# Kernel optimization log

Measured on AMD Instinct MI355X. Metric: run time of the kernel, lower is better.

Reference implementation:

```python
import jax, jax.numpy as jnp
import numpy as np

B, C, T, N = 8, 64, 24, 512
H = 2
D = C // H  # 32
NEG = -1e9
LN_EPS = 1e-5


def setup_inputs() -> dict:
    key = jax.random.key(0)
    ks = jax.random.split(key, 8)
    s = 1.0 / np.sqrt(C)
    return {
        "x": jax.random.normal(ks[0], (B, C, T, N), jnp.float32),
        "gso": jax.random.randint(ks[1], (N, N), 0, 2, jnp.int32),
        "Wq": jax.random.normal(ks[2], (C, C), jnp.float32) * s,
        "Wk": jax.random.normal(ks[3], (C, C), jnp.float32) * s,
        "Wv": jax.random.normal(ks[4], (C, C), jnp.float32) * s,
        "a_src": jax.random.normal(ks[5], (H, D), jnp.float32) * s,
        "a_dst": jax.random.normal(ks[6], (H, D), jnp.float32) * s,
        "gamma": jnp.ones((C,), jnp.float32),
        "beta": jnp.zeros((C,), jnp.float32),
    }


def reference(x, gso, Wq, Wk, Wv, a_src, a_dst, gamma, beta):
    # x: (B, C, T, N) -> (M, N, C) with M = B*T
    xr = jnp.transpose(x, (0, 2, 3, 1)).reshape(B * T, N, C)
    # torch Linear: y = x @ W.T ; split heads -> (M, N, H, D)
    Q = jnp.einsum('mnc,dc->mnd', xr, Wq).reshape(B * T, N, H, D)
    K = jnp.einsum('mnc,dc->mnd', xr, Wk).reshape(B * T, N, H, D)
    V = jnp.einsum('mnc,dc->mnd', xr, Wv).reshape(B * T, N, H, D)
    # additive GAT scores: s_ij = leaky_relu(<q_i, a_src> + <k_j, a_dst>)
    s_src = jnp.einsum('mnhd,hd->mhn', Q, a_src)  # (M, H, N)
    s_dst = jnp.einsum('mnhd,hd->mhn', K, a_dst)  # (M, H, N)
    scores = s_src[:, :, :, None] + s_dst[:, :, None, :]  # (M, H, N, N)
    scores = jax.nn.leaky_relu(scores, negative_slope=0.2)
    mask = jnp.where(gso == 0, jnp.float32(NEG), jnp.float32(0.0))  # (N, N)
    scores = scores + mask[None, None, :, :]
    attn = jax.nn.softmax(scores, axis=-1)  # dropout is identity in eval
    out = jnp.einsum('mhij,mjhd->mihd', attn, V).reshape(B * T, N, C)
    # LayerNorm over channels
    mu = jnp.mean(out, axis=-1, keepdims=True)
    var = jnp.var(out, axis=-1, keepdims=True)
    out = (out - mu) * jax.lax.rsqrt(var + LN_EPS) * gamma + beta
    # (M, N, C) -> (B, C, T, N)
    return jnp.transpose(out.reshape(B, T, N, C), (0, 3, 1, 2))
```

## Files before the change

### kernel.cpp

```cpp
#include <hip/hip_runtime.h>
#include <hip/hip_bf16.h>


#define NB 8
#define NC 64
#define NT 24
#define NN 512
#define NM 192
#define LOG2E 1.44269504088896f
#define NEGBIG -1.0e9f

typedef float f32x4 __attribute__((ext_vector_type(4)));
typedef short bf16x8 __attribute__((ext_vector_type(8)));
typedef int   i32x4 __attribute__((ext_vector_type(4)));
typedef unsigned int u32;
typedef u32 u32x2 __attribute__((ext_vector_type(2)));

#ifndef __has_builtin
#define __has_builtin(x) 0
#endif

__device__ __forceinline__ float fast_exp2(float x) {
#if __has_builtin(__builtin_amdgcn_exp2f)
    return __builtin_amdgcn_exp2f(x);
#else
    return exp2f(x);
#endif
}

__device__ __forceinline__ unsigned short f2bf(float f) {
    union { float f; unsigned int u; } v; v.f = f;
    unsigned int u = v.u;
    u += 0x7fffu + ((u >> 16) & 1u);
    return (unsigned short)(u >> 16);
}

__device__ __forceinline__ u32 pk_bf16(float lo, float hi) {
    __hip_bfloat162 h2 = __float22bfloat162_rn(float2{lo, hi});
    u32 r; __builtin_memcpy(&r, &h2, 4); return r;
}
__device__ __forceinline__ unsigned short f2bfh(float f) {
    __hip_bfloat16 h = __float2bfloat16(f);
    unsigned short r; __builtin_memcpy(&r, &h, 2); return r;
}

__device__ __forceinline__ float bf2f(unsigned short s) {
    union { unsigned int u; float f; } v;
    v.u = ((unsigned int)s) << 16;
    return v.f;
}

#define VT2_IDX(k2,h,qq,dt,dl,e) \
    ((((((k2)*2+(h))*4+(qq))*2+(dt))*16+(dl))*8+(e))

#define XRB(n,c) (((n)<<6) + (((((c)>>3) ^ ((n)&7))<<3) | ((c)&7)))

#define VT_IDX(h,k,qq,dt,dl,e) ((((((h)*16+(k))*4+(qq))*2+(dt))*16+(dl))*8+(e))

#define WS_VT_OFF   0u
#define WS_SSRC_OFF 12582912u
#define WS_SDST_OFF 13369344u
#define WS_MASK_OFF 14155776u
#define WS_NEEDED   15204352u

__global__ __launch_bounds__(512)
void gat_proj(const float* __restrict__ x, const int* __restrict__ gso,
              const float* __restrict__ Wq, const float* __restrict__ Wk,
              const float* __restrict__ Wv, const float* __restrict__ a_src,
              const float* __restrict__ a_dst,
              unsigned short* __restrict__ vt_ws, float* __restrict__ ssrc_ws,
              float* __restrict__ sdst_ws, float* __restrict__ mask_ws)
{
    __shared__ unsigned short sm_xrb[8192];
    __shared__ unsigned short sm_wvb[4096];
    __shared__ float sm_wqa[2][NC];
    __shared__ float sm_wka[2][NC];

    const int bid  = blockIdx.x;
    const int m    = bid >> 2;
    const int ch   = bid & 3;
    const int b    = m / NT;
    const int tt   = m % NT;
    const int tid  = threadIdx.x;
    const int lane = tid & 63;
    const int wid  = tid >> 6;
    const int fr   = lane & 15;
    const int fq   = lane >> 4;

    if (bid < 16) {
        const int w  = bid * 512 + tid;
        const int i  = w >> 4, kk = w & 15;
        const int* gp = &gso[i * NN + kk * 32];
        float* mp = &mask_ws[i * NN + kk * 32];
        #pragma unroll
        for (int q = 0; q < 8; ++q) {
            const i32x4 g = *reinterpret_cast<const i32x4*>(gp + q * 4);
            f32x4 f;
            #pragma unroll
            for (int e = 0; e < 4; ++e) f[e] = (g[e] != 0) ? 0.f : NEGBIG;
            *reinterpret_cast<f32x4*>(mp + q * 4) = f;
        }
    }

    if (tid < 128) {
        const int h = tid >> 6, c = tid & 63;
        float aq = 0.f, ak = 0.f;
        #pragma unroll
        for (int d = 0; d < 32; ++d) {
            aq += Wq[(h*32 + d)*NC + c] * a_src[h*32 + d];
            ak += Wk[(h*32 + d)*NC + c] * a_dst[h*32 + d];
        }
        sm_wqa[h][c] = aq * LOG2E;
        sm_wka[h][c] = ak * LOG2E;
    }
    for (int idx = tid; idx < 4096; idx += 512) {
        const int e   = idx & 7;
        const int dl  = (idx >> 3) & 15;
        const int dt4 = (idx >> 7) & 3;
        const int qq  = (idx >> 9) & 3;
        const int ks  = idx >> 11;
        sm_wvb[idx] = f2bfh(Wv[(dt4*16 + dl)*NC + ks*32 + qq*8 + e]);
    }

    const int nbase = ch * 128;

    {
        const int sl = tid & 127;
        const int sc = tid >> 7;
        #pragma unroll
        for (int half = 0; half < 2; ++half) {
            float v[8];
            #pragma unroll
            for (int e = 0; e < 8; ++e) {
                const int c = sc*16 + half*8 + e;
                v[e] = x[((size_t)(b*NC + c)*NT + tt)*NN + nbase + sl];
            }
            i32x4 w;
            #pragma unroll
            for (int j = 0; j < 4; ++j)
                w[j] = (int)pk_bf16(v[2*j], v[2*j+1]);
            *reinterpret_cast<i32x4*>(&sm_xrb[XRB(sl, sc*16 + half*8)]) = w;
        }
    }
    __syncthreads();

    {
        const int nl = tid >> 2;
        const int pp = tid & 3;
        float sq0=0.f, sq1=0.f, sk0=0.f, sk1=0.f;
        #pragma unroll
        for (int cc = 0; cc < 16; ++cc) {
            const int c = pp*16 + cc;
            const float xv = bf2f(sm_xrb[XRB(nl, c)]);
            sq0 += xv * sm_wqa[0][c];
            sq1 += xv * sm_wqa[1][c];
            sk0 += xv * sm_wka[0][c];
            sk1 += xv * sm_wka[1][c];
        }
        sq0 += __shfl_xor(sq0,1); sq0 += __shfl_xor(sq0,2);
        sq1 += __shfl_xor(sq1,1); sq1 += __shfl_xor(sq1,2);
        sk0 += __shfl_xor(sk0,1); sk0 += __shfl_xor(sk0,2);
        sk1 += __shfl_xor(sk1,1); sk1 += __shfl_xor(sk1,2);
        if (pp == 0) {
            ssrc_ws[((size_t)m*2 + 0)*NN + nbase + nl] = sq0;
            ssrc_ws[((size_t)m*2 + 1)*NN + nbase + nl] = sq1;
            sdst_ws[((size_t)m*2 + 0)*NN + nbase + nl] = sk0;
            sdst_ws[((size_t)m*2 + 1)*NN + nbase + nl] = sk1;
        }
    }

    {
        f32x4 vacc[4] = {};
        #pragma unroll
        for (int ks = 0; ks < 2; ++ks) {
            const bf16x8 af = *reinterpret_cast<const bf16x8*>(
                &sm_xrb[XRB(wid*16 + fr, ks*32 + fq*8)]);
            #pragma unroll
            for (int dt4 = 0; dt4 < 4; ++dt4) {
                const bf16x8 bfv = *reinterpret_cast<const bf16x8*>(
                    &sm_wvb[(((ks*4 + fq)*4 + dt4)*16 + fr)*8]);
                vacc[dt4] = __builtin_amdgcn_mfma_f32_16x16x32_bf16(
                    af, bfv, vacc[dt4], 0, 0, 0);
            }
        }
        const int n0 = nbase + wid*16 + 4*fq;
        #pragma unroll
        for (int dt4 = 0; dt4 < 4; ++dt4) {
            const int h = dt4 >> 1, dt = dt4 & 1;
            u32x2 dd;
            dd[0] = pk_bf16(vacc[dt4][0], vacc[dt4][1]);
            dd[1] = pk_bf16(vacc[dt4][2], vacc[dt4][3]);
            *reinterpret_cast<u32x2*>(
                &vt_ws[(size_t)m*32768 +
                       VT2_IDX(n0>>5, h, (n0>>3)&3, dt, fr, n0&7)]) = dd;
        }
    }
}

__global__ __launch_bounds__(512, 8)
void gat_attn(const unsigned short* __restrict__ vt_ws,
              const float* __restrict__ ssrc_ws, const float* __restrict__ sdst_ws,
              const float* __restrict__ mask_ws,
              const float* __restrict__ gamma, const float* __restrict__ beta,
              float* __restrict__ out)
{
    __shared__ unsigned short sm_vt[16384];
    __shared__ float sm_sdst[2][NN];
    __shared__ float sm_ssrc[2][128];

    const int bid  = blockIdx.x;
    const int m    = (bid >> 5) * 8 + (bid & 7);
    const int ch   = (bid >> 3) & 3;
    const int tid  = threadIdx.x;
    const int lane = tid & 63;
    const int wid  = tid >> 6;
    const int fr   = lane & 15;
    const int fq   = lane >> 4;

    const char* vsrc = (const char*)(vt_ws + (size_t)m * 32768);
#if __has_builtin(__builtin_amdgcn_global_load_lds)
    #pragma unroll
    for (int i = 0; i < 4; ++i) {
        __builtin_amdgcn_global_load_lds(
            (const __attribute__((address_space(1))) void*)
                (vsrc + i*8192 + tid*16),
            (__attribute__((address_space(3))) void*)
                (((__attribute__((address_space(3))) char*)sm_vt) +
                 i*8192 + (tid & ~63)*16),
            16, 0, 0);
    }
#else
    #pragma unroll
    for (int i = 0; i < 4; ++i) {
        reinterpret_cast<i32x4*>(sm_vt)[i*512 + tid] =
            reinterpret_cast<const i32x4*>(vsrc)[i*512 + tid];
    }
#endif
    if (tid < 256) {
        reinterpret_cast<f32x4*>(&sm_sdst[0][0])[tid] =
            reinterpret_cast<const f32x4*>(sdst_ws + (size_t)m*2*NN)[tid];
    } else {
        const int t = tid - 256;
        const int h = t >> 7, nloc = t & 127;
        sm_ssrc[h][nloc] = ssrc_ws[((size_t)m*2 + h)*NN + ch*128 + nloc];
    }
    __syncthreads();

    bf16x8 bones;
    {
        union { i32x4 i; bf16x8 h; } cv;
        const int w = (fr == 0) ? 0x3F803F80 : 0;
        cv.i[0] = w; cv.i[1] = w; cv.i[2] = w; cv.i[3] = w;
        bones = cv.h;
    }

    const int iloc = wid * 16;
    const int ig   = ch*128 + iloc + fr;
    const float src0 = sm_ssrc[0][iloc + fr];
    const float src1 = sm_ssrc[1][iloc + fr];
    const float* mrow = mask_ws + (size_t)ig * NN + fq*8;

    f32x4 acc[4] = {};
    f32x4 accs0 = {}, accs1 = {};

    #pragma unroll
    for (int hf = 0; hf < 2; ++hf) {
        #pragma unroll 4
        for (int k2 = 0; k2 < 8; ++k2) {
            const int k  = hf*8 + k2;
            const int j0 = k*32 + fq*8;
            const float* mp = mrow + k*32;
            const f32x4 ma = *reinterpret_cast<const f32x4*>(mp);
            const f32x4 mb = *reinterpret_cast<const f32x4*>(mp + 4);

            {
                const f32x4 da = *reinterpret_cast<const f32x4*>(&sm_sdst[0][j0]);
                const f32x4 db = *reinterpret_cast<const f32x4*>(&sm_sdst[0][j0+4]);
                u32 u[8];
                #pragma unroll
                for (int e = 0; e < 4; ++e) {
                    float sc = src0 + da[e] + ma[e];
                    sc = fmaxf(sc, 0.2f*sc);
                    u[e] = __float_as_uint(fast_exp2(sc));
                }
                #pragma unroll
                for (int e = 0; e < 4; ++e) {
                    float sc = src0 + db[e] + mb[e];
                    sc = fmaxf(sc, 0.2f*sc);
                    u[4+e] = __float_as_uint(fast_exp2(sc));
                }
                union { i32x4 i; bf16x8 h; } cv;
                cv.i[0] = __builtin_amdgcn_perm(u[1], u[0], 0x07060302u);
                cv.i[1] = __builtin_amdgcn_perm(u[3], u[2], 0x07060302u);
                cv.i[2] = __builtin_amdgcn_perm(u[5], u[4], 0x07060302u);
                cv.i[3] = __builtin_amdgcn_perm(u[7], u[6], 0x07060302u);
                const bf16x8 af = cv.h;
                accs0 = __builtin_amdgcn_mfma_f32_16x16x32_bf16(af, bones, accs0, 0,0,0);
                const bf16x8 b0 = *reinterpret_cast<const bf16x8*>(
                    &sm_vt[VT2_IDX(k2,0,fq,0,fr,0)]);
                const bf16x8 b1 = *reinterpret_cast<const bf16x8*>(
                    &sm_vt[VT2_IDX(k2,0,fq,1,fr,0)]);
                acc[0] = __builtin_amdgcn_mfma_f32_16x16x32_bf16(af, b0, acc[0], 0,0,0);
                acc[1] = __builtin_amdgcn_mfma_f32_16x16x32_bf16(af, b1, acc[1], 0,0,0);
            }
            {
                const f32x4 da = *reinterpret_cast<const f32x4*>(&sm_sdst[1][j0]);
                const f32x4 db = *reinterpret_cast<const f32x4*>(&sm_sdst[1][j0+4]);
                u32 u[8];
                #pragma unroll
                for (int e = 0; e < 4; ++e) {
                    float sc = src1 + da[e] + ma[e];
                    sc = fmaxf(sc, 0.2f*sc);
                    u[e] = __float_as_uint(fast_exp2(sc));
                }
                #pragma unroll
                for (int e = 0; e < 4; ++e) {
                    float sc = src1 + db[e] + mb[e];
                    sc = fmaxf(sc, 0.2f*sc);
                    u[4+e] = __float_as_uint(fast_exp2(sc));
                }
                union { i32x4 i; bf16x8 h; } cv;
                cv.i[0] = __builtin_amdgcn_perm(u[1], u[0], 0x07060302u);
                cv.i[1] = __builtin_amdgcn_perm(u[3], u[2], 0x07060302u);
                cv.i[2] = __builtin_amdgcn_perm(u[5], u[4], 0x07060302u);
                cv.i[3] = __builtin_amdgcn_perm(u[7], u[6], 0x07060302u);
                const bf16x8 af = cv.h;
                accs1 = __builtin_amdgcn_mfma_f32_16x16x32_bf16(af, bones, accs1, 0,0,0);
                const bf16x8 b0 = *reinterpret_cast<const bf16x8*>(
                    &sm_vt[VT2_IDX(k2,1,fq,0,fr,0)]);
                const bf16x8 b1 = *reinterpret_cast<const bf16x8*>(
                    &sm_vt[VT2_IDX(k2,1,fq,1,fr,0)]);
                acc[2] = __builtin_amdgcn_mfma_f32_16x16x32_bf16(af, b0, acc[2], 0,0,0);
                acc[3] = __builtin_amdgcn_mfma_f32_16x16x32_bf16(af, b1, acc[3], 0,0,0);
            }
        }

        if (hf == 0) {
            __syncthreads();
#if __has_builtin(__builtin_amdgcn_global_load_lds)
            #pragma unroll
            for (int i = 0; i < 4; ++i) {
                __builtin_amdgcn_global_load_lds(
                    (const __attribute__((address_space(1))) void*)
                        (vsrc + 32768 + i*8192 + tid*16),
                    (__attribute__((address_space(3))) void*)
                        (((__attribute__((address_space(3))) char*)sm_vt) +
                         i*8192 + (tid & ~63)*16),
                    16, 0, 0);
            }
#else
            #pragma unroll
            for (int i = 0; i < 4; ++i) {
                reinterpret_cast<i32x4*>(sm_vt)[i*512 + tid] =
                    reinterpret_cast<const i32x4*>(vsrc + 32768)[i*512 + tid];
            }
#endif
            __syncthreads();
        }
    }

    const int b_  = m / NT;
    const int tt  = m % NT;
    float gmv[4], btv[4];
    #pragma unroll
    for (int dt4 = 0; dt4 < 4; ++dt4) {
        gmv[dt4] = gamma[dt4*16 + fr];
        btv[dt4] = beta [dt4*16 + fr];
    }

    #pragma unroll
    for (int rg = 0; rg < 4; ++rg) {
        const int rowloc = 4*fq + rg;
        const float rs0 = __shfl(accs0[rg], lane & 48);
        const float rs1 = __shfl(accs1[rg], lane & 48);
        const float inv0 = 1.f / rs0, inv1 = 1.f / rs1;
        float vv[4];
        vv[0] = acc[0][rg] * inv0;
        vv[1] = acc[1][rg] * inv0;
        vv[2] = acc[2][rg] * inv1;
        vv[3] = acc[3][rg] * inv1;
        float sum = vv[0]+vv[1]+vv[2]+vv[3];
        float ssq = vv[0]*vv[0]+vv[1]*vv[1]+vv[2]*vv[2]+vv[3]*vv[3];
        sum += __shfl_xor(sum,1); sum += __shfl_xor(sum,2);
        sum += __shfl_xor(sum,4); sum += __shfl_xor(sum,8);
        ssq += __shfl_xor(ssq,1); ssq += __shfl_xor(ssq,2);
        ssq += __shfl_xor(ssq,4); ssq += __shfl_xor(ssq,8);
        const float mu   = sum * (1.f/64.f);
        const float var  = ssq * (1.f/64.f) - mu*mu;
        const float rstd = rsqrtf(var + 1e-5f);
        const int irow = ch*128 + iloc + rowloc;
        #pragma unroll
        for (int dt4 = 0; dt4 < 4; ++dt4) {
            const float o = (vv[dt4] - mu) * rstd * gmv[dt4] + btv[dt4];
            out[((size_t)(b_*NC + dt4*16 + fr)*NT + tt)*NN + irow] = o;
        }
    }
}

__global__ __launch_bounds__(512)
void gat_fused_mono(const float* __restrict__ x, const int* __restrict__ gso,
               const float* __restrict__ Wq, const float* __restrict__ Wk,
               const float* __restrict__ Wv, const float* __restrict__ a_src,
               const float* __restrict__ a_dst, const float* __restrict__ gamma,
               const float* __restrict__ beta, float* __restrict__ out)
{
    __shared__ unsigned short sm_xrb[128][72];
    __shared__ unsigned short sm_vt[32768];
    __shared__ unsigned short sm_wvb[4096];
    __shared__ float sm_ssrc[2][NN];
    __shared__ float sm_sdst[2][NN];
    __shared__ float sm_wqa[2][NC];
    __shared__ float sm_wka[2][NC];

    const int m    = blockIdx.x;
    const int b    = m / NT;
    const int tt   = m % NT;
    const int tid  = threadIdx.x;
    const int lane = tid & 63;
    const int wid  = tid >> 6;
    const int fr   = lane & 15;
    const int fq   = lane >> 4;

    if (tid < 128) {
        const int h = tid >> 6, c = tid & 63;
        float aq = 0.f, ak = 0.f;
        #pragma unroll
        for (int d = 0; d < 32; ++d) {
            aq += Wq[(h*32 + d)*NC + c] * a_src[h*32 + d];
            ak += Wk[(h*32 + d)*NC + c] * a_dst[h*32 + d];
        }
        sm_wqa[h][c] = aq;
        sm_wka[h][c] = ak;
    }
    for (int idx = tid; idx < 4096; idx += 512) {
        const int e   = idx & 7;
        const int dl  = (idx >> 3) & 15;
        const int dt4 = (idx >> 7) & 3;
        const int qq  = (idx >> 9) & 3;
        const int ks  = idx >> 11;
        sm_wvb[idx] = f2bf(Wv[(dt4*16 + dl)*NC + ks*32 + qq*8 + e]);
    }
    __syncthreads();

    const int nl = tid >> 2;
    const int pp = tid & 3;

    for (int ch = 0; ch < 4; ++ch) {
        const int nbase = ch * 128;
        #pragma unroll
        for (int half = 0; half < 2; ++half) {
            unsigned short tmp[8];
            #pragma unroll
            for (int e = 0; e < 8; ++e) {
                const int c = pp*16 + half*8 + e;
                tmp[e] = f2bf(x[((size_t)(b*NC + c)*NT + tt)*NN + nbase + nl]);
            }
            *reinterpret_cast<bf16x8*>(&sm_xrb[nl][pp*16 + half*8]) =
                *reinterpret_cast<const bf16x8*>(tmp);
        }
        __syncthreads();
        {
            float sq0=0.f, sq1=0.f, sk0=0.f, sk1=0.f;
            #pragma unroll
            for (int cc = 0; cc < 16; ++cc) {
                const int c = pp*16 + cc;
                const float xv = bf2f(sm_xrb[nl][c]);
                sq0 += xv * sm_wqa[0][c];
                sq1 += xv * sm_wqa[1][c];
                sk0 += xv * sm_wka[0][c];
                sk1 += xv * sm_wka[1][c];
            }
            sq0 += __shfl_xor(sq0,1); sq0 += __shfl_xor(sq0,2);
            sq1 += __shfl_xor(sq1,1); sq1 += __shfl_xor(sq1,2);
            sk0 += __shfl_xor(sk0,1); sk0 += __shfl_xor(sk0,2);
            sk1 += __shfl_xor(sk1,1); sk1 += __shfl_xor(sk1,2);
            if (pp == 0) {
                sm_ssrc[0][nbase+nl] = sq0;
                sm_ssrc[1][nbase+nl] = sq1;
                sm_sdst[0][nbase+nl] = sk0;
                sm_sdst[1][nbase+nl] = sk1;
            }
        }
        {
            f32x4 vacc[4] = {};
            #pragma unroll
            for (int ks = 0; ks < 2; ++ks) {
                const bf16x8 af = *reinterpret_cast<const bf16x8*>(
                    &sm_xrb[wid*16 + fr][ks*32 + fq*8]);
                #pragma unroll
                for (int dt4 = 0; dt4 < 4; ++dt4) {
                    const bf16x8 bfv = *reinterpret_cast<const bf16x8*>(
                        &sm_wvb[(((ks*4 + fq)*4 + dt4)*16 + fr)*8]);
                    vacc[dt4] = __builtin_amdgcn_mfma_f32_16x16x32_bf16(
                        af, bfv, vacc[dt4], 0, 0, 0);
                }
            }
            #pragma unroll
            for (int dt4 = 0; dt4 < 4; ++dt4) {
                const int h = dt4 >> 1, dt = dt4 & 1;
                #pragma unroll
                for (int rg = 0; rg < 4; ++rg) {
                    const int n = nbase + wid*16 + 4*fq + rg;
                    sm_vt[VT_IDX(h, n>>5, (n>>3)&3, dt, fr, n&7)] = f2bf(vacc[dt4][rg]);
                }
            }
        }
        __syncthreads();
    }

    float gmv[4], btv[4];
    #pragma unroll
    for (int dt4 = 0; dt4 < 4; ++dt4) {
        gmv[dt4] = gamma[dt4*16 + fr];
        btv[dt4] = beta [dt4*16 + fr];
    }

    for (int it = 0; it < 4; ++it) {
        const int ibase = (wid*4 + it) * 16;
        const int ig = ibase + fr;
        const float src0 = sm_ssrc[0][ig];
        const float src1 = sm_ssrc[1][ig];
        f32x4 acc[4] = {};
        float rsum0 = 0.f, rsum1 = 0.f;

        for (int k = 0; k < 16; ++k) {
            const int j0 = k*32 + fq*8;
            const int* gp = &gso[ig*NN + j0];
            const i32x4 g0 = *reinterpret_cast<const i32x4*>(gp);
            const i32x4 g1 = *reinterpret_cast<const i32x4*>(gp + 4);
            {
                const f32x4 da = *reinterpret_cast<const f32x4*>(&sm_sdst[0][j0]);
                const f32x4 db = *reinterpret_cast<const f32x4*>(&sm_sdst[0][j0+4]);
                bf16x8 af;
                #pragma unroll
                for (int e = 0; e < 4; ++e) {
                    float sc = src0 + da[e];
                    sc = fmaxf(sc, 0.2f*sc);
                    float ev = __expf(sc);
                    ev = (g0[e] != 0) ? ev : 0.f;
                    const unsigned short wb = f2bf(ev);
                    rsum0 += bf2f(wb);
                    af[e] = (short)wb;
                }
                #pragma unroll
                for (int e = 0; e < 4; ++e) {
                    float sc = src0 + db[e];
                    sc = fmaxf(sc, 0.2f*sc);
                    float ev = __expf(sc);
                    ev = (g1[e] != 0) ? ev : 0.f;
                    const unsigned short wb = f2bf(ev);
                    rsum0 += bf2f(wb);
                    af[4+e] = (short)wb;
                }
                const bf16x8 b0 = *reinterpret_cast<const bf16x8*>(&sm_vt[VT_IDX(0,k,fq,0,fr,0)]);
                const bf16x8 b1 = *reinterpret_cast<const bf16x8*>(&sm_vt[VT_IDX(0,k,fq,1,fr,0)]);
                acc[0] = __builtin_amdgcn_mfma_f32_16x16x32_bf16(af, b0, acc[0], 0,0,0);
                acc[1] = __builtin_amdgcn_mfma_f32_16x16x32_bf16(af, b1, acc[1], 0,0,0);
            }
            {
                const f32x4 da = *reinterpret_cast<const f32x4*>(&sm_sdst[1][j0]);
                const f32x4 db = *reinterpret_cast<const f32x4*>(&sm_sdst[1][j0+4]);
                bf16x8 af;
                #pragma unroll
                for (int e = 0; e < 4; ++e) {
                    float sc = src1 + da[e];
                    sc = fmaxf(sc, 0.2f*sc);
                    float ev = __expf(sc);
                    ev = (g0[e] != 0) ? ev : 0.f;
                    const unsigned short wb = f2bf(ev);
                    rsum1 += bf2f(wb);
                    af[e] = (short)wb;
                }
                #pragma unroll
                for (int e = 0; e < 4; ++e) {
                    float sc = src1 + db[e];
                    sc = fmaxf(sc, 0.2f*sc);
                    float ev = __expf(sc);
                    ev = (g1[e] != 0) ? ev : 0.f;
                    const unsigned short wb = f2bf(ev);
                    rsum1 += bf2f(wb);
                    af[4+e] = (short)wb;
                }
                const bf16x8 b0 = *reinterpret_cast<const bf16x8*>(&sm_vt[VT_IDX(1,k,fq,0,fr,0)]);
                const bf16x8 b1 = *reinterpret_cast<const bf16x8*>(&sm_vt[VT_IDX(1,k,fq,1,fr,0)]);
                acc[2] = __builtin_amdgcn_mfma_f32_16x16x32_bf16(af, b0, acc[2], 0,0,0);
                acc[3] = __builtin_amdgcn_mfma_f32_16x16x32_bf16(af, b1, acc[3], 0,0,0);
            }
        }

        rsum0 += __shfl_xor(rsum0, 16); rsum0 += __shfl_xor(rsum0, 32);
        rsum1 += __shfl_xor(rsum1, 16); rsum1 += __shfl_xor(rsum1, 32);

        #pragma unroll
        for (int rg = 0; rg < 4; ++rg) {
            const int rowloc   = 4*fq + rg;
            const int src_lane = (lane & 48) | rowloc;
            const float rs0 = __shfl(rsum0, src_lane);
            const float rs1 = __shfl(rsum1, src_lane);
            const float inv0 = 1.f / rs0, inv1 = 1.f / rs1;
            float vv[4];
            vv[0] = acc[0][rg] * inv0;
            vv[1] = acc[1][rg] * inv0;
            vv[2] = acc[2][rg] * inv1;
            vv[3] = acc[3][rg] * inv1;
            float sum = vv[0]+vv[1]+vv[2]+vv[3];
            float ssq = vv[0]*vv[0]+vv[1]*vv[1]+vv[2]*vv[2]+vv[3]*vv[3];
            sum += __shfl_xor(sum,1); sum += __shfl_xor(sum,2);
            sum += __shfl_xor(sum,4); sum += __shfl_xor(sum,8);
            ssq += __shfl_xor(ssq,1); ssq += __shfl_xor(ssq,2);
            ssq += __shfl_xor(ssq,4); ssq += __shfl_xor(ssq,8);
            const float mu   = sum * (1.f/64.f);
            const float var  = ssq * (1.f/64.f) - mu*mu;
            const float rstd = rsqrtf(var + 1e-5f);
            const int irow = ibase + rowloc;
            #pragma unroll
            for (int dt4 = 0; dt4 < 4; ++dt4) {
                const float o = (vv[dt4] - mu) * rstd * gmv[dt4] + btv[dt4];
                out[((size_t)(b*NC + dt4*16 + fr)*NT + tt)*NN + irow] = o;
            }
        }
    }
}

extern "C" void kernel_launch(void* const* d_in, const int* in_sizes, int n_in,
                              void* d_out, int out_size, void* d_ws, size_t ws_size,
                              hipStream_t stream) {
    (void)in_sizes; (void)n_in; (void)out_size;
    const float* x     = (const float*)d_in[0];
    const int*   gso   = (const int*)  d_in[1];
    const float* Wq    = (const float*)d_in[2];
    const float* Wk    = (const float*)d_in[3];
    const float* Wv    = (const float*)d_in[4];
    const float* a_src = (const float*)d_in[5];
    const float* a_dst = (const float*)d_in[6];
    const float* gamma = (const float*)d_in[7];
    const float* beta  = (const float*)d_in[8];
    float* out = (float*)d_out;

    if (ws_size >= (size_t)WS_NEEDED && d_ws != nullptr) {
        unsigned short* vt = (unsigned short*)((char*)d_ws + WS_VT_OFF);
        float* ssrc  = (float*)((char*)d_ws + WS_SSRC_OFF);
        float* sdst  = (float*)((char*)d_ws + WS_SDST_OFF);
        float* maskf = (float*)((char*)d_ws + WS_MASK_OFF);
        gat_proj<<<768, 512, 0, stream>>>(x, gso, Wq, Wk, Wv, a_src, a_dst,
                                          vt, ssrc, sdst, maskf);
        gat_attn<<<768, 512, 0, stream>>>(vt, ssrc, sdst, maskf, gamma, beta, out);
    } else {
        gat_fused_mono<<<NM, 512, 0, stream>>>(x, gso, Wq, Wk, Wv, a_src, a_dst,
                                               gamma, beta, out);
    }
}
```

Baseline: 52.43 us.

## Factor exp of leaky-relu scores into per-node exponentials and read gso directly

Uses exp2(leaky(a+b)) = max(exp2(a)exp2(b), exp2(0.2a)exp2(0.2b)), so the projection kernel stores exponentiated source and destination terms and the attention inner loop needs only multiplies and a max instead of a per-pair exp. The mask precompute in the projection kernel is dropped; the attention kernel reads the int adjacency directly and zeroes masked weights with a select. This removes transcendental work from the N×N loop at the cost of doubled per-node score buffers, more LDS, lower occupancy bounds, and no max-subtraction, so exp2 of large scores could overflow.

After: 50.38 us. -3.9%, faster.

```diff
diff --git a/kernel.cpp b/kernel.cpp
--- a/kernel.cpp
+++ b/kernel.cpp
@@ -8,7 +8,6 @@
 #define NN 512
 #define NM 192
 #define LOG2E 1.44269504088896f
-#define NEGBIG -1.0e9f
 
 typedef float f32x4 __attribute__((ext_vector_type(4)));
 typedef short bf16x8 __attribute__((ext_vector_type(8)));
@@ -43,7 +42,6 @@
     __hip_bfloat16 h = __float2bfloat16(f);
     unsigned short r; __builtin_memcpy(&r, &h, 2); return r;
 }
-
 __device__ __forceinline__ float bf2f(unsigned short s) {
     union { unsigned int u; float f; } v;
     v.u = ((unsigned int)s) << 16;
@@ -59,17 +57,16 @@
 
 #define WS_VT_OFF   0u
 #define WS_SSRC_OFF 12582912u
-#define WS_SDST_OFF 13369344u
-#define WS_MASK_OFF 14155776u
-#define WS_NEEDED   15204352u
+#define WS_SDST_OFF 14155776u
+#define WS_NEEDED   15728640u
 
 __global__ __launch_bounds__(512)
-void gat_proj(const float* __restrict__ x, const int* __restrict__ gso,
+void gat_proj(const float* __restrict__ x,
               const float* __restrict__ Wq, const float* __restrict__ Wk,
               const float* __restrict__ Wv, const float* __restrict__ a_src,
               const float* __restrict__ a_dst,
               unsigned short* __restrict__ vt_ws, float* __restrict__ ssrc_ws,
-              float* __restrict__ sdst_ws, float* __restrict__ mask_ws)
+              float* __restrict__ sdst_ws)
 {
     __shared__ unsigned short sm_xrb[8192];
     __shared__ unsigned short sm_wvb[4096];
@@ -87,21 +84,6 @@
     const int fr   = lane & 15;
     const int fq   = lane >> 4;
 
-    if (bid < 16) {
-        const int w  = bid * 512 + tid;
-        const int i  = w >> 4, kk = w & 15;
-        const int* gp = &gso[i * NN + kk * 32];
-        float* mp = &mask_ws[i * NN + kk * 32];
-        #pragma unroll
-        for (int q = 0; q < 8; ++q) {
-            const i32x4 g = *reinterpret_cast<const i32x4*>(gp + q * 4);
-            f32x4 f;
-            #pragma unroll
-            for (int e = 0; e < 4; ++e) f[e] = (g[e] != 0) ? 0.f : NEGBIG;
-            *reinterpret_cast<f32x4*>(mp + q * 4) = f;
-        }
-    }
-
     if (tid < 128) {
         const int h = tid >> 6, c = tid & 63;
         float aq = 0.f, ak = 0.f;
@@ -162,10 +144,17 @@
         sk0 += __shfl_xor(sk0,1); sk0 += __shfl_xor(sk0,2);
         sk1 += __shfl_xor(sk1,1); sk1 += __shfl_xor(sk1,2);
         if (pp == 0) {
-            ssrc_ws[((size_t)m*2 + 0)*NN + nbase + nl] = sq0;
-            ssrc_ws[((size_t)m*2 + 1)*NN + nbase + nl] = sq1;
-            sdst_ws[((size_t)m*2 + 0)*NN + nbase + nl] = sk0;
-            sdst_ws[((size_t)m*2 + 1)*NN + nbase + nl] = sk1;
+            const int n = nbase + nl;
+            float* sb = ssrc_ws + (size_t)m*4*NN;
+            float* db = sdst_ws + (size_t)m*4*NN;
+            sb[0*NN + n] = fast_exp2(sq0);
+            sb[1*NN + n] = fast_exp2(0.2f*sq0);
+            sb[2*NN + n] = fast_exp2(sq1);
+            sb[3*NN + n] = fast_exp2(0.2f*sq1);
+            db[0*NN + n] = fast_exp2(sk0);
+            db[1*NN + n] = fast_exp2(0.2f*sk0);
+            db[2*NN + n] = fast_exp2(sk1);
+            db[3*NN + n] = fast_exp2(0.2f*sk1);
         }
     }
 
@@ -197,16 +186,16 @@
     }
 }
 
-__global__ __launch_bounds__(512, 8)
+__global__ __launch_bounds__(512, 6)
 void gat_attn(const unsigned short* __restrict__ vt_ws,
               const float* __restrict__ ssrc_ws, const float* __restrict__ sdst_ws,
-              const float* __restrict__ mask_ws,
+              const int* __restrict__ gso,
               const float* __restrict__ gamma, const float* __restrict__ beta,
               float* __restrict__ out)
 {
     __shared__ unsigned short sm_vt[16384];
-    __shared__ float sm_sdst[2][NN];
-    __shared__ float sm_ssrc[2][128];
+    __shared__ float sm_F[2][2][NN];
+    __shared__ float sm_E[2][2][128];
 
     const int bid  = blockIdx.x;
     const int m    = (bid >> 5) * 8 + (bid & 7);
@@ -236,13 +225,12 @@
             reinterpret_cast<const i32x4*>(vsrc)[i*512 + tid];
     }
 #endif
-    if (tid < 256) {
-        reinterpret_cast<f32x4*>(&sm_sdst[0][0])[tid] =
-            reinterpret_cast<const f32x4*>(sdst_ws + (size_t)m*2*NN)[tid];
-    } else {
-        const int t = tid - 256;
-        const int h = t >> 7, nloc = t & 127;
-        sm_ssrc[h][nloc] = ssrc_ws[((size_t)m*2 + h)*NN + ch*128 + nloc];
+    reinterpret_cast<f32x4*>(&sm_F[0][0][0])[tid] =
+        reinterpret_cast<const f32x4*>(sdst_ws + (size_t)m*4*NN)[tid];
+    {
+        const int h = tid >> 8, v = (tid >> 7) & 1, nloc = tid & 127;
+        sm_E[h][v][nloc] =
+            ssrc_ws[((size_t)m*4 + h*2 + v)*NN + ch*128 + nloc];
     }
     __syncthreads();
 
@@ -256,38 +244,38 @@
 
     const int iloc = wid * 16;
     const int ig   = ch*128 + iloc + fr;
-    const float src0 = sm_ssrc[0][iloc + fr];
-    const float src1 = sm_ssrc[1][iloc + fr];
-    const float* mrow = mask_ws + (size_t)ig * NN + fq*8;
+    const float Ei0  = sm_E[0][0][iloc + fr];
+    const float Ei0p = sm_E[0][1][iloc + fr];
+    const float Ei1  = sm_E[1][0][iloc + fr];
+    const float Ei1p = sm_E[1][1][iloc + fr];
+    const int* grow = gso + (size_t)ig * NN + fq*8;
 
     f32x4 acc[4] = {};
     f32x4 accs0 = {}, accs1 = {};
 
     #pragma unroll
     for (int hf = 0; hf < 2; ++hf) {
-        #pragma unroll 4
         for (int k2 = 0; k2 < 8; ++k2) {
             const int k  = hf*8 + k2;
             const int j0 = k*32 + fq*8;
-            const float* mp = mrow + k*32;
-            const f32x4 ma = *reinterpret_cast<const f32x4*>(mp);
-            const f32x4 mb = *reinterpret_cast<const f32x4*>(mp + 4);
+            const i32x4 g0 = *reinterpret_cast<const i32x4*>(grow + k*32);
+            const i32x4 g1 = *reinterpret_cast<const i32x4*>(grow + k*32 + 4);
 
             {
-                const f32x4 da = *reinterpret_cast<const f32x4*>(&sm_sdst[0][j0]);
-                const f32x4 db = *reinterpret_cast<const f32x4*>(&sm_sdst[0][j0+4]);
+                const f32x4 Fa = *reinterpret_cast<const f32x4*>(&sm_F[0][0][j0]);
+                const f32x4 Fb = *reinterpret_cast<const f32x4*>(&sm_F[0][0][j0+4]);
+                const f32x4 Pa = *reinterpret_cast<const f32x4*>(&sm_F[0][1][j0]);
+                const f32x4 Pb = *reinterpret_cast<const f32x4*>(&sm_F[0][1][j0+4]);
                 u32 u[8];
                 #pragma unroll
                 for (int e = 0; e < 4; ++e) {
-                    float sc = src0 + da[e] + ma[e];
-                    sc = fmaxf(sc, 0.2f*sc);
-                    u[e] = __float_as_uint(fast_exp2(sc));
-                }
-                #pragma unroll
-                for (int e = 0; e < 4; ++e) {
-                    float sc = src0 + db[e] + mb[e];
-                    sc = fmaxf(sc, 0.2f*sc);
-                    u[4+e] = __float_as_uint(fast_exp2(sc));
+                    const float w = fmaxf(Ei0*Fa[e], Ei0p*Pa[e]);
+                    u[e] = (g0[e] != 0) ? __float_as_uint(w) : 0u;
+                }
+                #pragma unroll
+                for (int e = 0; e < 4; ++e) {
+                    const float w = fmaxf(Ei0*Fb[e], Ei0p*Pb[e]);
+                    u[4+e] = (g1[e] != 0) ? __float_as_uint(w) : 0u;
                 }
                 union { i32x4 i; bf16x8 h; } cv;
                 cv.i[0] = __builtin_amdgcn_perm(u[1], u[0], 0x07060302u);
@@ -304,20 +292,20 @@
                 acc[1] = __builtin_amdgcn_mfma_f32_16x16x32_bf16(af, b1, acc[1], 0,0,0);
             }
             {
-                const f32x4 da = *reinterpret_cast<const f32x4*>(&sm_sdst[1][j0]);
-                const f32x4 db = *reinterpret_cast<const f32x4*>(&sm_sdst[1][j0+4]);
+                const f32x4 Fa = *reinterpret_cast<const f32x4*>(&sm_F[1][0][j0]);
+                const f32x4 Fb = *reinterpret_cast<const f32x4*>(&sm_F[1][0][j0+4]);
+                const f32x4 Pa = *reinterpret_cast<const f32x4*>(&sm_F[1][1][j0]);
+                const f32x4 Pb = *reinterpret_cast<const f32x4*>(&sm_F[1][1][j0+4]);
                 u32 u[8];
                 #pragma unroll
                 for (int e = 0; e < 4; ++e) {
-                    float sc = src1 + da[e] + ma[e];
-                    sc = fmaxf(sc, 0.2f*sc);
-                    u[e] = __float_as_uint(fast_exp2(sc));
-                }
-                #pragma unroll
-                for (int e = 0; e < 4; ++e) {
-                    float sc = src1 + db[e] + mb[e];
-                    sc = fmaxf(sc, 0.2f*sc);
-                    u[4+e] = __float_as_uint(fast_exp2(sc));
+                    const float w = fmaxf(Ei1*Fa[e], Ei1p*Pa[e]);
+                    u[e] = (g0[e] != 0) ? __float_as_uint(w) : 0u;
+                }
+                #pragma unroll
+                for (int e = 0; e < 4; ++e) {
+                    const float w = fmaxf(Ei1*Fb[e], Ei1p*Pb[e]);
+                    u[4+e] = (g1[e] != 0) ? __float_as_uint(w) : 0u;
                 }
                 union { i32x4 i; bf16x8 h; } cv;
                 cv.i[0] = __builtin_amdgcn_perm(u[1], u[0], 0x07060302u);
@@ -641,10 +629,10 @@
         unsigned short* vt = (unsigned short*)((char*)d_ws + WS_VT_OFF);
         float* ssrc  = (float*)((char*)d_ws + WS_SSRC_OFF);
         float* sdst  = (float*)((char*)d_ws + WS_SDST_OFF);
-        float* maskf = (float*)((char*)d_ws + WS_MASK_OFF);
-        gat_proj<<<768, 512, 0, stream>>>(x, gso, Wq, Wk, Wv, a_src, a_dst,
-                                          vt, ssrc, sdst, maskf);
-        gat_attn<<<768, 512, 0, stream>>>(vt, ssrc, sdst, maskf, gamma, beta, out);
+        gat_proj<<<768, 512, 0, stream>>>(x, Wq, Wk, Wv, a_src, a_dst,
+                                          vt, ssrc, sdst);
+        gat_attn<<<768, 512, 0, stream>>>(vt, ssrc, sdst, gso,
+                                          gamma, beta, out);
     } else {
         gat_fused_mono<<<NM, 512, 0, stream>>>(x, gso, Wq, Wk, Wv, a_src, a_dst,
                                                gamma, beta, out);
```
